# Kernel tuning notes

Measured on AMD Instinct MI355X. Metric: run time of the kernel, lower is better.

Reference implementation:

```python
import jax, jax.numpy as jnp
import numpy as np

N, E, IN, OUT = 50000, 1600000, 128, 64
BN_EPS = 1e-5


def setup_inputs() -> dict:
    key = jax.random.key(0)
    ks = jax.random.split(key, 12)
    x = jax.random.normal(ks[0], (N, IN), jnp.float32)
    edge_index = jax.random.randint(ks[1], (2, E), 0, N)
    node_embeddings = jax.random.normal(ks[2], (N, OUT), jnp.float32)
    W = jax.random.normal(ks[3], (OUT, IN), jnp.float32) / np.sqrt(IN).astype(np.float32)
    att_i = jax.random.normal(ks[4], (OUT,), jnp.float32) * 0.1
    att_j = jax.random.normal(ks[5], (OUT,), jnp.float32) * 0.1
    att_em_i = jax.random.normal(ks[6], (OUT,), jnp.float32) * 0.1
    att_em_j = jax.random.normal(ks[7], (OUT,), jnp.float32) * 0.1
    bias = jax.random.normal(ks[8], (OUT,), jnp.float32) * 0.01
    gamma = jnp.ones((OUT,), jnp.float32)
    beta = jnp.zeros((OUT,), jnp.float32)
    return dict(x=x, edge_index=edge_index, node_embeddings=node_embeddings, W=W,
                att_i=att_i, att_j=att_j, att_em_i=att_em_i, att_em_j=att_em_j,
                bias=bias, gamma=gamma, beta=beta)


def _segment_softmax(logits, seg, num_segments):
    # numerically stable softmax over edges grouped by destination node
    m = jax.ops.segment_max(logits, seg, num_segments=num_segments)
    e = jnp.exp(logits - m[seg])
    s = jax.ops.segment_sum(e, seg, num_segments=num_segments)
    return e / (s[seg] + 1e-16)


def reference(x, edge_index, node_embeddings, W, att_i, att_j, att_em_i, att_em_j,
              bias, gamma, beta):
    n = x.shape[0]
    h = x @ W.T                                  # [N, OUT] linear projection
    src, dst = edge_index[0], edge_index[1]      # j -> i (source_to_target)
    # per-node attention scalars first (N*OUT work), then gather scalars per edge
    # (same math as gathering [E,OUT] keys, far less memory traffic)
    a_i = h @ att_i + node_embeddings @ att_em_i  # [N]
    a_j = h @ att_j + node_embeddings @ att_em_j  # [N]
    logits = jax.nn.leaky_relu(a_i[dst] + a_j[src], 0.2)   # [E]
    alpha = _segment_softmax(logits, dst, n)                # [E]
    agg = jax.ops.segment_sum(h[src] * alpha[:, None], dst, num_segments=n)  # [N, OUT]
    out = agg + bias
    # BatchNorm1d (training mode: batch stats, biased variance) + ReLU
    mean = out.mean(0)
    var = out.var(0)
    y = gamma * (out - mean) * jax.lax.rsqrt(var + BN_EPS) + beta
    return jax.nn.relu(y)
```

## Files before the change

kernel.cpp:

```cpp
#include <hip/hip_runtime.h>
#include <climits>

#define NN 50000
#define EE 1600000
#define DIN 128
#define DOUT 64
#define BN_EPS 1e-5f

#define NPB 32
#define NB  1563
#define CAPB 1536
#define KA_WGS 512
#define KA_CHUNK (EE / KA_WGS)

__global__ void k0_init(int* gcur, float* colsum, float* colsq) {
    int i = blockIdx.x * blockDim.x + threadIdx.x;
    if (i < NB) gcur[i] = 0;
    if (i < DOUT) { colsum[i] = 0.f; colsq[i] = 0.f; }
}

__global__ void k1_gemm(const float* __restrict__ x, const float* __restrict__ W,
                        const float* __restrict__ ne,
                        const float* __restrict__ atti, const float* __restrict__ attj,
                        const float* __restrict__ atemi, const float* __restrict__ atemj,
                        float* __restrict__ h, float* __restrict__ a_i, float* __restrict__ a_j) {
    const int l = threadIdx.x & 63;
    const int wv = threadIdx.x >> 6;
    const int gw = blockIdx.x * (blockDim.x >> 6) + wv;
    const int nw = gridDim.x * (blockDim.x >> 6);

    float4 w4[32];
    const float4* Wv = (const float4*)(W + l * DIN);
#pragma unroll
    for (int j = 0; j < 32; ++j) w4[j] = Wv[j];

    const float ai_l = atti[l], aj_l = attj[l], emi_l = atemi[l], emj_l = atemj[l];

    for (int n = gw; n < NN; n += nw) {
        const float4* xv = (const float4*)(x + n * DIN);
        float acc = 0.f;
#pragma unroll
        for (int j = 0; j < 32; ++j) {
            float4 xx = xv[j];
            acc += w4[j].x * xx.x + w4[j].y * xx.y + w4[j].z * xx.z + w4[j].w * xx.w;
        }
        float nev = ne[n * DOUT + l];
        float v1 = acc * ai_l + nev * emi_l;
        float v2 = acc * aj_l + nev * emj_l;
#pragma unroll
        for (int d = 32; d >= 1; d >>= 1) {
            v1 += __shfl_xor(v1, d);
            v2 += __shfl_xor(v2, d);
        }
        h[n * DOUT + l] = acc;
        if (l == 0) { a_i[n] = v1; a_j[n] = v2; }
    }
}

__global__ void __launch_bounds__(256) kA_bin(const int* __restrict__ ei,
                                              int* __restrict__ gcur,
                                              unsigned int* __restrict__ binned) {
    __shared__ int hist[NB];
    __shared__ int base_l[NB];
    __shared__ unsigned int recs[KA_CHUNK];
    const int t = threadIdx.x;
    for (int i = t; i < NB; i += 256) hist[i] = 0;
    __syncthreads();
    const int e0 = blockIdx.x * KA_CHUNK;
    for (int e = e0 + t; e < e0 + KA_CHUNK; e += 256) {
        int src = ei[e];
        int dst = ei[EE + e];
        atomicAdd(&hist[dst >> 5], 1);
        recs[e - e0] = (unsigned)src | ((unsigned)dst << 16);
    }
    __syncthreads();
    for (int b = t; b < NB; b += 256) {
        int c = hist[b];
        base_l[b] = c > 0 ? atomicAdd(&gcur[b], c) : 0;
        hist[b] = 0;
    }
    __syncthreads();
    for (int e = e0 + t; e < e0 + KA_CHUNK; e += 256) {
        unsigned r = recs[e - e0];
        int dst = r >> 16;
        int b = dst >> 5;
        int pos = base_l[b] + atomicAdd(&hist[b], 1);
        binned[b * CAPB + pos] = (r & 0xffffu) | ((unsigned)(dst & 31) << 16);
    }
}

__global__ void __launch_bounds__(256) kB_agg(const unsigned int* __restrict__ binned,
                                              const int* __restrict__ gcur,
                                              const float* __restrict__ h,
                                              const float* __restrict__ a_i,
                                              const float* __restrict__ a_j,
                                              const float* __restrict__ bias,
                                              float* __restrict__ out_pre,
                                              float* __restrict__ colsum,
                                              float* __restrict__ colsq) {
    __shared__ float agg[NPB * DOUT];
    __shared__ float s_l[NPB];
    __shared__ float ai_l[NPB];
    const int b = blockIdx.x;
    const int node0 = b * NPB;
    const int nlocal = min(NPB, NN - node0);
    const int t = threadIdx.x;
    const int l = t & 63, wv = t >> 6;
    const float bias_l = bias[l];

    for (int i = t; i < NPB * DOUT; i += 256) agg[i] = 0.f;
    if (t < NPB) {
        s_l[t] = 0.f;
        ai_l[t] = (t < nlocal) ? a_i[node0 + t] : 0.f;
    }
    __syncthreads();

    const int cnt = gcur[b];
    const unsigned int* bin = binned + b * CAPB;

    for (int base = wv * 64; base < cnt; base += 256) {
        const int kk = min(64, cnt - base);
        unsigned r = (l < kk) ? bin[base + l] : 0u;
        int src = r & 0xffffu;
        int dl = (r >> 16) & 31;
        float ev = 0.f;
        if (l < kk) {
            float lg = ai_l[dl] + a_j[src];
            lg = lg > 0.f ? lg : 0.2f * lg;
            ev = __expf(lg);
            atomicAdd(&s_l[dl], ev);
        }
        int evi = __float_as_int(ev);
        if (kk == 64) {
#pragma unroll
            for (int kb = 0; kb < 64; kb += 16) {
                float hv[16];
                float evb[16];
                int   db[16];
#pragma unroll
                for (int u = 0; u < 16; ++u) {
                    int k = kb + u;
                    int sK = __builtin_amdgcn_readlane(src, k);
                    db[u] = __builtin_amdgcn_readlane(dl, k);
                    evb[u] = __int_as_float(__builtin_amdgcn_readlane(evi, k));
                    hv[u] = h[(sK << 6) + l];
                }
#pragma unroll
                for (int u = 0; u < 16; ++u)
                    atomicAdd(&agg[(db[u] << 6) + l], evb[u] * hv[u]);
            }
        } else {
            for (int k = 0; k < kk; ++k) {
                int sK = __builtin_amdgcn_readlane(src, k);
                int dK = __builtin_amdgcn_readlane(dl, k);
                float eK = __int_as_float(__builtin_amdgcn_readlane(evi, k));
                float hvv = h[(sK << 6) + l];
                atomicAdd(&agg[(dK << 6) + l], eK * hvv);
            }
        }
    }
    __syncthreads();

    float bsum = 0.f, bsq = 0.f;
    for (int j = wv; j < nlocal; j += 4) {
        float v = agg[j * 64 + l] / (s_l[j] + 1e-16f) + bias_l;
        out_pre[(node0 + j) * 64 + l] = v;
        bsum += v;
        bsq += v * v;
    }
    __syncthreads();
    agg[wv * 64 + l] = bsum;
    agg[256 + wv * 64 + l] = bsq;
    __syncthreads();
    if (wv == 0) {
        float ts = agg[l] + agg[64 + l] + agg[128 + l] + agg[192 + l];
        float tq = agg[256 + l] + agg[320 + l] + agg[384 + l] + agg[448 + l];
        atomicAdd(&colsum[l], ts);
        atomicAdd(&colsq[l], tq);
    }
}

__global__ void k6_coef(const float* __restrict__ colsum, const float* __restrict__ colsq,
                        const float* __restrict__ gamma, const float* __restrict__ beta,
                        float* __restrict__ scale, float* __restrict__ shift) {
    int c = threadIdx.x;
    if (c < DOUT) {
        float mean = colsum[c] * (1.f / NN);
        float var = colsq[c] * (1.f / NN) - mean * mean;
        float inv = rsqrtf(var + BN_EPS);
        float sc = gamma[c] * inv;
        scale[c] = sc;
        shift[c] = beta[c] - mean * sc;
    }
}

__global__ void k7_apply(const float4* __restrict__ out_pre,
                         const float4* __restrict__ scale, const float4* __restrict__ shift,
                         float4* __restrict__ y) {
    const int n4 = NN * DOUT / 4;
    int tid = blockIdx.x * blockDim.x + threadIdx.x;
    int stride = gridDim.x * blockDim.x;
    for (int i = tid; i < n4; i += stride) {
        float4 o = out_pre[i];
        int c = i & 15;
        float4 sc = scale[c], sh = shift[c];
        float4 r;
        r.x = fmaxf(o.x * sc.x + sh.x, 0.f);
        r.y = fmaxf(o.y * sc.y + sh.y, 0.f);
        r.z = fmaxf(o.z * sc.z + sh.z, 0.f);
        r.w = fmaxf(o.w * sc.w + sh.w, 0.f);
        y[i] = r;
    }
}

extern "C" void kernel_launch(void* const* d_in, const int* in_sizes, int n_in,
                              void* d_out, int out_size, void* d_ws, size_t ws_size,
                              hipStream_t stream) {
    const float* x      = (const float*)d_in[0];
    const int*   ei     = (const int*)d_in[1];
    const float* ne     = (const float*)d_in[2];
    const float* W      = (const float*)d_in[3];
    const float* att_i  = (const float*)d_in[4];
    const float* att_j  = (const float*)d_in[5];
    const float* atemi  = (const float*)d_in[6];
    const float* atemj  = (const float*)d_in[7];
    const float* bias   = (const float*)d_in[8];
    const float* gamma  = (const float*)d_in[9];
    const float* beta   = (const float*)d_in[10];
    float* out = (float*)d_out;

    char* w = (char*)d_ws;
    size_t off = 0;
    auto alloc = [&](size_t bytes) -> void* {
        void* p = w + off;
        off = (off + bytes + 255) & ~(size_t)255;
        return p;
    };
    float*        h       = (float*)alloc((size_t)NN * DOUT * 4);
    float*        out_pre = (float*)alloc((size_t)NN * DOUT * 4);
    unsigned int* binned  = (unsigned int*)alloc((size_t)NB * CAPB * 4);
    float*        a_i     = (float*)alloc((size_t)NN * 4);
    float*        a_j     = (float*)alloc((size_t)NN * 4);
    int*          gcur    = (int*)alloc((size_t)NB * 4);
    float*        colsum  = (float*)alloc(DOUT * 4);
    float*        colsq   = (float*)alloc(DOUT * 4);
    float*        scale   = (float*)alloc(DOUT * 4);
    float*        shift   = (float*)alloc(DOUT * 4);

    k0_init<<<(NB + 255) / 256, 256, 0, stream>>>(gcur, colsum, colsq);
    k1_gemm<<<1024, 256, 0, stream>>>(x, W, ne, att_i, att_j, atemi, atemj, h, a_i, a_j);
    kA_bin<<<KA_WGS, 256, 0, stream>>>(ei, gcur, binned);
    kB_agg<<<NB, 256, 0, stream>>>(binned, gcur, h, a_i, a_j, bias, out_pre, colsum, colsq);
    k6_coef<<<1, 64, 0, stream>>>(colsum, colsq, gamma, beta, scale, shift);
    k7_apply<<<1024, 256, 0, stream>>>((const float4*)out_pre, (const float4*)scale,
                                       (const float4*)shift, (float4*)out);
}
```

Before: 889.9 us.

## Split edge binning into coarse and fine passes, batch all 64 gathers

Replaces the single-pass binning of edges into 1563 fine destination bins with two passes. A coarse pass buckets edges into 49 groups of 1024 nodes, reusing the out_pre buffer as scratch. A fine pass then splits each group into 32 bins. This cuts per-block histogram size and reduces scattered global writes and atomics. The aggregation kernel also issues all 64 h-row gathers before any shared atomics, behind a sched_barrier, which raises memory-level parallelism at the cost of 64 extra registers per lane and possible occupancy loss.

New measurement: 878.3 us. Within noise of the previous version (-1.3%).

```diff
diff --git a/kernel.cpp b/kernel.cpp
--- a/kernel.cpp
+++ b/kernel.cpp
@@ -10,12 +10,16 @@
 #define NPB 32
 #define NB  1563
 #define CAPB 1536
-#define KA_WGS 512
-#define KA_CHUNK (EE / KA_WGS)
-
-__global__ void k0_init(int* gcur, float* colsum, float* colsq) {
+#define NCB 49
+#define CAPC 35200
+#define KA1_WGS 512
+#define KA1_CHUNK (EE / KA1_WGS)
+#define KA2_SPLIT 16
+
+__global__ void k0_init(int* gcur, int* gcurC, float* colsum, float* colsq) {
     int i = blockIdx.x * blockDim.x + threadIdx.x;
-    if (i < NB) gcur[i] = 0;
+    if (i < NB + 8) gcur[i] = 0;
+    if (i < NCB) gcurC[i] = 0;
     if (i < DOUT) { colsum[i] = 0.f; colsq[i] = 0.f; }
 }
 
@@ -57,35 +61,70 @@
     }
 }
 
-__global__ void __launch_bounds__(256) kA_bin(const int* __restrict__ ei,
-                                              int* __restrict__ gcur,
-                                              unsigned int* __restrict__ binned) {
-    __shared__ int hist[NB];
-    __shared__ int base_l[NB];
-    __shared__ unsigned int recs[KA_CHUNK];
+__global__ void __launch_bounds__(256) kA1_coarse(const int* __restrict__ ei,
+                                                  int* __restrict__ gcurC,
+                                                  unsigned int* __restrict__ coarse) {
+    __shared__ int hist[NCB];
+    __shared__ int base_l[NCB];
+    __shared__ unsigned int recs[KA1_CHUNK];
     const int t = threadIdx.x;
-    for (int i = t; i < NB; i += 256) hist[i] = 0;
-    __syncthreads();
-    const int e0 = blockIdx.x * KA_CHUNK;
-    for (int e = e0 + t; e < e0 + KA_CHUNK; e += 256) {
+    if (t < NCB) hist[t] = 0;
+    __syncthreads();
+    const int e0 = blockIdx.x * KA1_CHUNK;
+    for (int e = e0 + t; e < e0 + KA1_CHUNK; e += 256) {
         int src = ei[e];
         int dst = ei[EE + e];
-        atomicAdd(&hist[dst >> 5], 1);
+        atomicAdd(&hist[dst >> 10], 1);
         recs[e - e0] = (unsigned)src | ((unsigned)dst << 16);
     }
     __syncthreads();
-    for (int b = t; b < NB; b += 256) {
-        int c = hist[b];
-        base_l[b] = c > 0 ? atomicAdd(&gcur[b], c) : 0;
-        hist[b] = 0;
-    }
-    __syncthreads();
-    for (int e = e0 + t; e < e0 + KA_CHUNK; e += 256) {
+    if (t < NCB) {
+        int c = hist[t];
+        base_l[t] = c > 0 ? atomicAdd(&gcurC[t], c) : 0;
+        hist[t] = 0;
+    }
+    __syncthreads();
+    for (int e = e0 + t; e < e0 + KA1_CHUNK; e += 256) {
         unsigned r = recs[e - e0];
-        int dst = r >> 16;
-        int b = dst >> 5;
-        int pos = base_l[b] + atomicAdd(&hist[b], 1);
-        binned[b * CAPB + pos] = (r & 0xffffu) | ((unsigned)(dst & 31) << 16);
+        int cb = (r >> 16) >> 10;
+        int pos = base_l[cb] + atomicAdd(&hist[cb], 1);
+        coarse[cb * CAPC + pos] = r;
+    }
+}
+
+__global__ void __launch_bounds__(256) kA2_fine(const unsigned int* __restrict__ coarse,
+                                                const int* __restrict__ gcurC,
+                                                int* __restrict__ gcur,
+                                                unsigned int* __restrict__ binned) {
+    __shared__ int hist[32];
+    __shared__ int base_l[32];
+    __shared__ unsigned int recs[CAPC / KA2_SPLIT + 64];
+    const int c = blockIdx.x >> 4;
+    const int q = blockIdx.x & 15;
+    const int len = gcurC[c];
+    const int start = (len * q) / KA2_SPLIT;
+    const int end = (len * (q + 1)) / KA2_SPLIT;
+    const int t = threadIdx.x;
+    if (t < 32) hist[t] = 0;
+    __syncthreads();
+    const unsigned int* cb = coarse + c * CAPC;
+    for (int i = start + t; i < end; i += 256) {
+        unsigned r = cb[i];
+        recs[i - start] = r;
+        atomicAdd(&hist[(r >> 21) & 31], 1);
+    }
+    __syncthreads();
+    if (t < 32) {
+        int n = hist[t];
+        base_l[t] = n > 0 ? atomicAdd(&gcur[c * 32 + t], n) : 0;
+        hist[t] = 0;
+    }
+    __syncthreads();
+    for (int i = start + t; i < end; i += 256) {
+        unsigned r = recs[i - start];
+        int fb = (r >> 21) & 31;
+        int pos = base_l[fb] + atomicAdd(&hist[fb], 1);
+        binned[(c * 32 + fb) * CAPB + pos] = (r & 0xffffu) | (((r >> 16) & 31u) << 16);
     }
 }
 
@@ -132,22 +171,18 @@
         }
         int evi = __float_as_int(ev);
         if (kk == 64) {
-#pragma unroll
-            for (int kb = 0; kb < 64; kb += 16) {
-                float hv[16];
-                float evb[16];
-                int   db[16];
-#pragma unroll
-                for (int u = 0; u < 16; ++u) {
-                    int k = kb + u;
-                    int sK = __builtin_amdgcn_readlane(src, k);
-                    db[u] = __builtin_amdgcn_readlane(dl, k);
-                    evb[u] = __int_as_float(__builtin_amdgcn_readlane(evi, k));
-                    hv[u] = h[(sK << 6) + l];
-                }
-#pragma unroll
-                for (int u = 0; u < 16; ++u)
-                    atomicAdd(&agg[(db[u] << 6) + l], evb[u] * hv[u]);
+            float hv[64];
+#pragma unroll
+            for (int u = 0; u < 64; ++u) {
+                int sK = __builtin_amdgcn_readlane(src, u);
+                hv[u] = h[(sK << 6) + l];
+            }
+            __builtin_amdgcn_sched_barrier(0);
+#pragma unroll
+            for (int u = 0; u < 64; ++u) {
+                int dK = __builtin_amdgcn_readlane(dl, u);
+                float eK = __int_as_float(__builtin_amdgcn_readlane(evi, u));
+                atomicAdd(&agg[(dK << 6) + l], eK * hv[u]);
             }
         } else {
             for (int k = 0; k < kk; ++k) {
@@ -241,15 +276,18 @@
     unsigned int* binned  = (unsigned int*)alloc((size_t)NB * CAPB * 4);
     float*        a_i     = (float*)alloc((size_t)NN * 4);
     float*        a_j     = (float*)alloc((size_t)NN * 4);
-    int*          gcur    = (int*)alloc((size_t)NB * 4);
+    int*          gcur    = (int*)alloc((size_t)(NB + 8) * 4);
+    int*          gcurC   = (int*)alloc((size_t)NCB * 4);
     float*        colsum  = (float*)alloc(DOUT * 4);
     float*        colsq   = (float*)alloc(DOUT * 4);
     float*        scale   = (float*)alloc(DOUT * 4);
     float*        shift   = (float*)alloc(DOUT * 4);
-
-    k0_init<<<(NB + 255) / 256, 256, 0, stream>>>(gcur, colsum, colsq);
+    unsigned int* coarse  = (unsigned int*)out_pre;
+
+    k0_init<<<(NB + 255 + 8) / 256, 256, 0, stream>>>(gcur, gcurC, colsum, colsq);
     k1_gemm<<<1024, 256, 0, stream>>>(x, W, ne, att_i, att_j, atemi, atemj, h, a_i, a_j);
-    kA_bin<<<KA_WGS, 256, 0, stream>>>(ei, gcur, binned);
+    kA1_coarse<<<KA1_WGS, 256, 0, stream>>>(ei, gcurC, coarse);
+    kA2_fine<<<NCB * KA2_SPLIT, 256, 0, stream>>>(coarse, gcurC, gcur, binned);
     kB_agg<<<NB, 256, 0, stream>>>(binned, gcur, h, a_i, a_j, bias, out_pre, colsum, colsq);
     k6_coef<<<1, 64, 0, stream>>>(colsum, colsq, gamma, beta, scale, shift);
     k7_apply<<<1024, 256, 0, stream>>>((const float4*)out_pre, (const float4*)scale,
```
